# Optimization experiments

Measured on AMD Instinct MI355X. Metric: run time of the kernel, lower is better.

## Reference

```python
import jax, jax.numpy as jnp
import numpy as np

WS = 6          # window size
NUM_HEADS = 6
HEAD_DIM = 32   # dim=192 / 6 heads
SCALE = HEAD_DIM ** -0.5


def _rel_pos_index(ws):
    # Faithful to the torch buffer construction (torch.meshgrid default 'ij').
    coords = np.stack(np.meshgrid(np.arange(ws), np.arange(ws), np.arange(ws), indexing='ij'))  # [3,ws,ws,ws]
    flat = coords.reshape(3, -1)                       # [3, ws^3]
    rel = flat[:, :, None] - flat[:, None, :]          # [3, N, N]
    rel = rel.transpose(1, 2, 0).astype(np.int64)      # [N, N, 3]
    rel += ws - 1
    rel[..., 0] *= 3 * ws - 1
    rel[..., 1] *= 2 * ws - 1
    return rel.sum(-1)                                 # [N, N]

REL_INDEX = jnp.asarray(_rel_pos_index(WS))            # [216, 216] int


def setup_inputs() -> dict:
    key = jax.random.key(0)
    k1, k2, k3, k4 = jax.random.split(key, 4)
    B, N, C = 1024, WS ** 3, NUM_HEADS * HEAD_DIM
    return {
        "x": jax.random.normal(k1, (B, N, C), dtype=jnp.float32),
        "qkv_w": jax.random.normal(k2, (3 * C, C), dtype=jnp.float32) * 0.02,
        "proj_w": jax.random.normal(k3, (C, C), dtype=jnp.float32) * 0.02,
        "proj_b": jnp.zeros((C,), dtype=jnp.float32),
        "bias_table": jax.random.normal(k4, ((2 * WS - 1) ** 3, NUM_HEADS), dtype=jnp.float32) * 0.02,
    }


def reference(x, qkv_w, proj_w, proj_b, bias_table):
    B, N, C = x.shape
    H, D = NUM_HEADS, HEAD_DIM
    qkv = jnp.einsum('bnc,fc->bnf', x, qkv_w)              # [B,N,3C]
    qkv = qkv.reshape(B, N, 3, H, D).transpose(2, 0, 3, 1, 4)  # [3,B,H,N,D]
    q, k, v = qkv[0], qkv[1], qkv[2]
    attn = jnp.einsum('bhnd,bhmd->bhnm', q * SCALE, k)     # [B,H,N,N]
    bias = bias_table[REL_INDEX]                           # [N,N,H]
    attn = attn + bias.transpose(2, 0, 1)[None]            # add [1,H,N,N]
    attn = jax.nn.softmax(attn, axis=-1)
    out = jnp.einsum('bhnm,bhmd->bhnd', attn, v)           # [B,H,N,D]
    out = out.transpose(0, 2, 1, 3).reshape(B, N, C)
    return jnp.einsum('bnc,oc->bno', out, proj_w) + proj_b
```

## Files before the change

### kernel.cpp

```cpp
#include <hip/hip_runtime.h>
#include <cstdint>
#include <cstddef>


typedef __attribute__((ext_vector_type(8))) short short8;
typedef __attribute__((ext_vector_type(4))) float f32x4;

#define SCALE_F 0.17677669529663687f

__device__ __forceinline__ unsigned short f2bf(float f) {
  union { float f; unsigned u; } v; v.f = f;
  return (unsigned short)((v.u + 0x7fffu + ((v.u >> 16) & 1u)) >> 16);
}

__device__ __forceinline__ f32x4 mfma16(short8 a, short8 b, f32x4 c) {
  return __builtin_amdgcn_mfma_f32_16x16x32_bf16(a, b, c, 0, 0, 0);
}

__global__ void prep_kernel(const float* __restrict__ qkv_w,
                            const float* __restrict__ proj_w,
                            const float* __restrict__ bias_table,
                            unsigned short* __restrict__ wb,
                            unsigned short* __restrict__ pwb,
                            float* __restrict__ biasg) {
  const int tid = blockIdx.x * blockDim.x + threadIdx.x;
  const int stride = gridDim.x * blockDim.x;
  for (int i = tid; i < 576 * 192; i += stride) wb[i] = f2bf(qkv_w[i]);
  for (int i = tid; i < 192 * 192; i += stride) pwb[i] = f2bf(proj_w[i]);
  for (int i = tid; i < 6 * 216 * 216; i += stride) {
    const int h = i / 46656, rem = i % 46656;
    const int n = rem / 216, m = rem % 216;
    const int di = n / 36 - m / 36;
    const int dj = (n / 6) % 6 - (m / 6) % 6;
    const int dk = n % 6 - m % 6;
    const int idx = (di + 5) * 17 + (dj + 5) * 11 + (dk + 5);
    biasg[i] = bias_table[idx * 6 + h];
  }
}

__global__ __launch_bounds__(1024, 4)
void attn_kernel(const float* __restrict__ x, const unsigned short* __restrict__ wb,
                 const float* __restrict__ biasg, float* __restrict__ outbuf) {
  extern __shared__ char smem[];
  unsigned short* xs  = (unsigned short*)(smem);
  unsigned short* qs  = (unsigned short*)(smem + 86400);
  unsigned short* ks  = (unsigned short*)(smem + 104320);
  unsigned short* vT  = (unsigned short*)(smem + 122240);
  unsigned short* pch = (unsigned short*)(smem + 137088);

  const int b = blockIdx.x;
  const int tid = threadIdx.x;
  const int wave = tid >> 6;
  const int lane = tid & 63;
  const int quad = lane >> 4;
  const int lcol = lane & 15;

  {
    const float4* xg4 = (const float4*)(x + (size_t)b * 41472);
    for (int i = tid; i < 216 * 48; i += 1024) {
      const int row = i / 48, c4 = i % 48;
      const float4 v = xg4[row * 48 + c4];
      union { unsigned short s[4]; unsigned long long u; } pk;
      pk.s[0] = f2bf(v.x); pk.s[1] = f2bf(v.y);
      pk.s[2] = f2bf(v.z); pk.s[3] = f2bf(v.w);
      *(unsigned long long*)(xs + row * 200 + c4 * 4) = pk.u;
    }
    for (int i = tid; i < 8 * 40; i += 1024) { qs[216 * 40 + i] = 0; ks[216 * 40 + i] = 0; }
    for (int i = tid; i < 32 * 8; i += 1024) vT[(i >> 3) * 232 + 216 + (i & 7)] = 0;
  }
  __syncthreads();

  unsigned short* attnb = (unsigned short*)(outbuf + (size_t)b * 41472);

  for (int h = 0; h < 6; ++h) {
    for (int u = wave; u < 14; u += 16) {
      const int mtp = u >> 1;
      const int nh  = u & 1;
      f32x4 acc[2][3] = {};
#pragma unroll
      for (int kk = 0; kk < 6; ++kk) {
        const short8 a0 = *(const short8*)(xs + (mtp * 32      + lcol) * 200 + kk * 32 + quad * 8);
        const short8 a1 = *(const short8*)(xs + (mtp * 32 + 16 + lcol) * 200 + kk * 32 + quad * 8);
#pragma unroll
        for (int j = 0; j < 3; ++j) {
          const int nt = nh * 3 + j;
          const int fbase = (nt >> 1) * 192 + h * 32 + (nt & 1) * 16;
          const short8 bf = *(const short8*)(wb + (fbase + lcol) * 192 + kk * 32 + quad * 8);
          acc[0][j] = mfma16(a0, bf, acc[0][j]);
          acc[1][j] = mfma16(a1, bf, acc[1][j]);
        }
      }
#pragma unroll
      for (int mi = 0; mi < 2; ++mi) {
        const int nbase = (mtp * 2 + mi) * 16 + quad * 4;
#pragma unroll
        for (int j = 0; j < 3; ++j) {
          const int nt = nh * 3 + j;
#pragma unroll
          for (int r = 0; r < 4; ++r) {
            const int n = nbase + r;
            if (n < 216) {
              const unsigned short val = f2bf(acc[mi][j][r]);
              if (nt < 2)      qs[n * 40 + (nt & 1) * 16 + lcol] = val;
              else if (nt < 4) ks[n * 40 + (nt & 1) * 16 + lcol] = val;
              else             vT[((nt & 1) * 16 + lcol) * 232 + n] = val;
            }
          }
        }
      }
    }
    __syncthreads();

    if (wave < 14) {
      const int s = wave;
      unsigned short* pw_ = pch + wave * 640;
      const short8 qa = *(const short8*)(qs + (s * 16 + lcol) * 40 + quad * 8);
      f32x4 o0 = {}, o1 = {}, rsum = {};
      for (int mt2 = 0; mt2 < 7; ++mt2) {
        const short8 kb0 = *(const short8*)(ks + (mt2 * 32      + lcol) * 40 + quad * 8);
        const short8 kb1 = *(const short8*)(ks + (mt2 * 32 + 16 + lcol) * 40 + quad * 8);
        const f32x4 zero = {};
        const f32x4 s0 = mfma16(qa, kb0, zero);
        const f32x4 s1 = mfma16(qa, kb1, zero);
        const int nb = s * 16 + quad * 4;
#pragma unroll
        for (int t = 0; t < 2; ++t) {
          const int m = mt2 * 32 + t * 16 + lcol;
#pragma unroll
          for (int r = 0; r < 4; ++r) {
            const int n = nb + r;
            const int nc = (n < 216) ? n : 0;
            float p = 0.0f;
            if (m < 216)
              p = __expf((t ? s1[r] : s0[r]) * SCALE_F + biasg[(h * 216 + nc) * 216 + m]);
            rsum[r] += p;
            pw_[(quad * 4 + r) * 40 + t * 16 + lcol] = f2bf(p);
          }
        }
        __builtin_amdgcn_s_waitcnt(0);
        const short8 pa  = *(const short8*)(pw_ + lcol * 40 + quad * 8);
        const short8 vb0 = *(const short8*)(vT + lcol * 232        + mt2 * 32 + quad * 8);
        const short8 vb1 = *(const short8*)(vT + (16 + lcol) * 232 + mt2 * 32 + quad * 8);
        o0 = mfma16(pa, vb0, o0);
        o1 = mfma16(pa, vb1, o1);
      }
      f32x4 inv;
#pragma unroll
      for (int r = 0; r < 4; ++r) {
        float ssum = rsum[r];
        ssum += __shfl_xor(ssum, 1, 16);
        ssum += __shfl_xor(ssum, 2, 16);
        ssum += __shfl_xor(ssum, 4, 16);
        ssum += __shfl_xor(ssum, 8, 16);
        inv[r] = 1.0f / ssum;
      }
#pragma unroll
      for (int t = 0; t < 2; ++t) {
#pragma unroll
        for (int r = 0; r < 4; ++r) {
          const int n = s * 16 + quad * 4 + r;
          if (n < 216)
            attnb[n * 192 + h * 32 + t * 16 + lcol] = f2bf((t ? o1[r] : o0[r]) * inv[r]);
        }
      }
    }
    __syncthreads();
  }
}

__global__ __launch_bounds__(512, 2)
void proj_kernel(const unsigned short* __restrict__ pw, const float* __restrict__ proj_b,
                 float* __restrict__ outbuf) {
  extern __shared__ char smem[];
  unsigned short* as = (unsigned short*)smem;
  const int b = blockIdx.x, tid = threadIdx.x;
  const int wave = tid >> 6, lane = tid & 63, quad = lane >> 4, lcol = lane & 15;
  float* myout = outbuf + (size_t)b * 41472;
  const unsigned short* attnb = (const unsigned short*)myout;

  for (int i = tid; i < 216 * 24; i += 512) {
    const int row = i / 24, c8 = i % 24;
    *(short8*)(as + row * 200 + c8 * 8) = *(const short8*)(attnb + row * 192 + c8 * 8);
  }
  __syncthreads();

  for (int u = wave; u < 14; u += 8) {
    short8 a[6];
#pragma unroll
    for (int kk = 0; kk < 6; ++kk)
      a[kk] = *(const short8*)(as + (u * 16 + lcol) * 200 + kk * 32 + quad * 8);
    for (int nt = 0; nt < 12; ++nt) {
      f32x4 acc = {};
#pragma unroll
      for (int kk = 0; kk < 6; ++kk) {
        const short8 bf = *(const short8*)(pw + (nt * 16 + lcol) * 192 + kk * 32 + quad * 8);
        acc = mfma16(a[kk], bf, acc);
      }
      const float pbv = proj_b[nt * 16 + lcol];
      const int nb = u * 16 + quad * 4;
#pragma unroll
      for (int r = 0; r < 4; ++r) {
        const int n = nb + r;
        if (n < 216) myout[n * 192 + nt * 16 + lcol] = acc[r] + pbv;
      }
    }
  }
}

extern "C" void kernel_launch(void* const* d_in, const int* in_sizes, int n_in,
                              void* d_out, int out_size, void* d_ws, size_t ws_size,
                              hipStream_t stream) {
  (void)in_sizes; (void)n_in; (void)out_size; (void)ws_size;
  const float* x          = (const float*)d_in[0];
  const float* qkv_w      = (const float*)d_in[1];
  const float* proj_w     = (const float*)d_in[2];
  const float* proj_b     = (const float*)d_in[3];
  const float* bias_table = (const float*)d_in[4];
  float* out = (float*)d_out;

  unsigned short* wb  = (unsigned short*)d_ws;
  unsigned short* pwb = (unsigned short*)((char*)d_ws + 221184);
  float* biasg        = (float*)((char*)d_ws + 294912);

  (void)hipFuncSetAttribute((const void*)attn_kernel,
                            hipFuncAttributeMaxDynamicSharedMemorySize, 157568);
  (void)hipFuncSetAttribute((const void*)proj_kernel,
                            hipFuncAttributeMaxDynamicSharedMemorySize, 89600);

  prep_kernel<<<dim3(256), dim3(256), 0, stream>>>(qkv_w, proj_w, bias_table, wb, pwb, biasg);
  attn_kernel<<<dim3(1024), dim3(1024), 157568, stream>>>(x, wb, biasg, out);
  proj_kernel<<<dim3(1024), dim3(512), 89600, stream>>>(pwb, proj_b, out);
}
```

Measured before the change: 929.2 us.

## Pack bias as bf16 in MFMA layout, restructure QKV tiling and stage proj weights

Precomputes the relative position bias as bf16 in a layout that matches the MFMA output fragment, with masked columns set to -inf. Each attention wave can then load its bias with a few vector loads instead of many scattered fp32 gathers and skip the bounds checks. The QKV projection now uses one 16-row tile per wave with six output tiles and packed 32-bit stores, and V columns are permuted so P·V reads line up. The projection kernel stages its bf16 weights in padded LDS and runs with 1024 threads. Rounding the bias to bf16 adds a small precision loss, and the larger LDS use may lower occupancy.

Result: faster. 811.7 us (-12.6%).

```diff
diff --git a/kernel.cpp b/kernel.cpp
--- a/kernel.cpp
+++ b/kernel.cpp
@@ -5,12 +5,25 @@
 
 typedef __attribute__((ext_vector_type(8))) short short8;
 typedef __attribute__((ext_vector_type(4))) float f32x4;
+typedef unsigned short u16;
+typedef unsigned int   u32;
 
 #define SCALE_F 0.17677669529663687f
 
-__device__ __forceinline__ unsigned short f2bf(float f) {
-  union { float f; unsigned u; } v; v.f = f;
-  return (unsigned short)((v.u + 0x7fffu + ((v.u >> 16) & 1u)) >> 16);
+#define XS_OFF   0
+#define QS_OFF   89600
+#define KS_OFF   107520
+#define VT_OFF   125440
+#define PCH_OFF  140288
+#define ATTN_LDS 158208
+
+#define PROJ_AS_OFF  0
+#define PROJ_PW_OFF  86400
+#define PROJ_LDS     163200
+
+__device__ __forceinline__ u16 f2bf(float f) {
+  union { float f; u32 u; } v; v.f = f;
+  return (u16)((v.u + 0x7fffu + ((v.u >> 16) & 1u)) >> 16);
 }
 
 __device__ __forceinline__ f32x4 mfma16(short8 a, short8 b, f32x4 c) {
@@ -20,33 +33,44 @@
 __global__ void prep_kernel(const float* __restrict__ qkv_w,
                             const float* __restrict__ proj_w,
                             const float* __restrict__ bias_table,
-                            unsigned short* __restrict__ wb,
-                            unsigned short* __restrict__ pwb,
-                            float* __restrict__ biasg) {
+                            u16* __restrict__ wb,
+                            u16* __restrict__ pwb,
+                            u16* __restrict__ biasp) {
   const int tid = blockIdx.x * blockDim.x + threadIdx.x;
   const int stride = gridDim.x * blockDim.x;
   for (int i = tid; i < 576 * 192; i += stride) wb[i] = f2bf(qkv_w[i]);
   for (int i = tid; i < 192 * 192; i += stride) pwb[i] = f2bf(proj_w[i]);
-  for (int i = tid; i < 6 * 216 * 216; i += stride) {
-    const int h = i / 46656, rem = i % 46656;
-    const int n = rem / 216, m = rem % 216;
-    const int di = n / 36 - m / 36;
-    const int dj = (n / 6) % 6 - (m / 6) % 6;
-    const int dk = n % 6 - m % 6;
-    const int idx = (di + 5) * 17 + (dj + 5) * 11 + (dk + 5);
-    biasg[i] = bias_table[idx * 6 + h];
+  for (int i = tid; i < 6 * 7 * 16 * 224 * 2; i += stride) {
+    const int t = i & 1;
+    int j = i >> 1;
+    const int n = j % 224; j /= 224;
+    const int l = j & 15;  j >>= 4;
+    const int c = j % 7;
+    const int h = j / 7;
+    const int m = c * 32 + t * 16 + l;
+    u16 val;
+    if (n >= 216)      val = 0;
+    else if (m >= 216) val = 0xFF80;
+    else {
+      const int di = n / 36 - m / 36;
+      const int dj = (n / 6) % 6 - (m / 6) % 6;
+      const int dk = n % 6 - m % 6;
+      const int idx = (di + 5) * 17 + (dj + 5) * 11 + (dk + 5);
+      val = f2bf(bias_table[idx * 6 + h]);
+    }
+    biasp[i] = val;
   }
 }
 
 __global__ __launch_bounds__(1024, 4)
-void attn_kernel(const float* __restrict__ x, const unsigned short* __restrict__ wb,
-                 const float* __restrict__ biasg, float* __restrict__ outbuf) {
+void attn_kernel(const float* __restrict__ x, const u16* __restrict__ wb,
+                 const u16* __restrict__ biasp, float* __restrict__ outbuf) {
   extern __shared__ char smem[];
-  unsigned short* xs  = (unsigned short*)(smem);
-  unsigned short* qs  = (unsigned short*)(smem + 86400);
-  unsigned short* ks  = (unsigned short*)(smem + 104320);
-  unsigned short* vT  = (unsigned short*)(smem + 122240);
-  unsigned short* pch = (unsigned short*)(smem + 137088);
+  u16* xs  = (u16*)(smem + XS_OFF);
+  u16* qs  = (u16*)(smem + QS_OFF);
+  u16* ks  = (u16*)(smem + KS_OFF);
+  u16* vT  = (u16*)(smem + VT_OFF);
+  u16* pch = (u16*)(smem + PCH_OFF);
 
   const int b = blockIdx.x;
   const int tid = threadIdx.x;
@@ -60,52 +84,46 @@
     for (int i = tid; i < 216 * 48; i += 1024) {
       const int row = i / 48, c4 = i % 48;
       const float4 v = xg4[row * 48 + c4];
-      union { unsigned short s[4]; unsigned long long u; } pk;
+      union { u16 s[4]; unsigned long long u; } pk;
       pk.s[0] = f2bf(v.x); pk.s[1] = f2bf(v.y);
       pk.s[2] = f2bf(v.z); pk.s[3] = f2bf(v.w);
       *(unsigned long long*)(xs + row * 200 + c4 * 4) = pk.u;
     }
     for (int i = tid; i < 8 * 40; i += 1024) { qs[216 * 40 + i] = 0; ks[216 * 40 + i] = 0; }
-    for (int i = tid; i < 32 * 8; i += 1024) vT[(i >> 3) * 232 + 216 + (i & 7)] = 0;
+    for (int i = tid; i < 32 * 8; i += 1024) {
+      const int d = i >> 3, jj = i & 7;
+      vT[d * 232 + 209 + 2 * jj] = 0;
+    }
   }
   __syncthreads();
 
-  unsigned short* attnb = (unsigned short*)(outbuf + (size_t)b * 41472);
+  u16* attnb = (u16*)(outbuf + (size_t)b * 41472);
 
   for (int h = 0; h < 6; ++h) {
     for (int u = wave; u < 14; u += 16) {
-      const int mtp = u >> 1;
-      const int nh  = u & 1;
-      f32x4 acc[2][3] = {};
+      f32x4 acc[6] = {};
 #pragma unroll
       for (int kk = 0; kk < 6; ++kk) {
-        const short8 a0 = *(const short8*)(xs + (mtp * 32      + lcol) * 200 + kk * 32 + quad * 8);
-        const short8 a1 = *(const short8*)(xs + (mtp * 32 + 16 + lcol) * 200 + kk * 32 + quad * 8);
-#pragma unroll
-        for (int j = 0; j < 3; ++j) {
-          const int nt = nh * 3 + j;
-          const int fbase = (nt >> 1) * 192 + h * 32 + (nt & 1) * 16;
+        const short8 a = *(const short8*)(xs + (u * 16 + lcol) * 200 + kk * 32 + quad * 8);
+#pragma unroll
+        for (int j = 0; j < 6; ++j) {
+          const int fbase = (j >> 1) * 192 + h * 32 + (j & 1) * 16;
           const short8 bf = *(const short8*)(wb + (fbase + lcol) * 192 + kk * 32 + quad * 8);
-          acc[0][j] = mfma16(a0, bf, acc[0][j]);
-          acc[1][j] = mfma16(a1, bf, acc[1][j]);
-        }
-      }
-#pragma unroll
-      for (int mi = 0; mi < 2; ++mi) {
-        const int nbase = (mtp * 2 + mi) * 16 + quad * 4;
-#pragma unroll
-        for (int j = 0; j < 3; ++j) {
-          const int nt = nh * 3 + j;
-#pragma unroll
-          for (int r = 0; r < 4; ++r) {
-            const int n = nbase + r;
-            if (n < 216) {
-              const unsigned short val = f2bf(acc[mi][j][r]);
-              if (nt < 2)      qs[n * 40 + (nt & 1) * 16 + lcol] = val;
-              else if (nt < 4) ks[n * 40 + (nt & 1) * 16 + lcol] = val;
-              else             vT[((nt & 1) * 16 + lcol) * 232 + n] = val;
-            }
-          }
+          acc[j] = mfma16(a, bf, acc[j]);
+        }
+      }
+      const int nb = u * 16 + quad * 4;
+#pragma unroll
+      for (int r = 0; r < 4; ++r) {
+        const int n = nb + r;
+        if (n < 216) {
+          *(u32*)(qs + n * 40 + 2 * lcol) =
+              (u32)f2bf(acc[0][r]) | ((u32)f2bf(acc[1][r]) << 16);
+          *(u32*)(ks + n * 40 + 2 * lcol) =
+              (u32)f2bf(acc[2][r]) | ((u32)f2bf(acc[3][r]) << 16);
+          const int pm = (n & ~31) | (2 * (n & 15)) | ((n >> 4) & 1);
+          vT[lcol * 232 + pm]        = f2bf(acc[4][r]);
+          vT[(16 + lcol) * 232 + pm] = f2bf(acc[5][r]);
         }
       }
     }
@@ -113,37 +131,51 @@
 
     if (wave < 14) {
       const int s = wave;
-      unsigned short* pw_ = pch + wave * 640;
+      u16* pw_ = pch + wave * 640;
+
+      uint4 bias_q[7];
+#pragma unroll
+      for (int c = 0; c < 7; ++c)
+        bias_q[c] = *(const uint4*)(biasp + ((size_t)((h * 7 + c) * 16 + lcol)) * 448
+                                    + (s * 16 + quad * 4) * 2);
       const short8 qa = *(const short8*)(qs + (s * 16 + lcol) * 40 + quad * 8);
-      f32x4 o0 = {}, o1 = {}, rsum = {};
-      for (int mt2 = 0; mt2 < 7; ++mt2) {
-        const short8 kb0 = *(const short8*)(ks + (mt2 * 32      + lcol) * 40 + quad * 8);
-        const short8 kb1 = *(const short8*)(ks + (mt2 * 32 + 16 + lcol) * 40 + quad * 8);
-        const f32x4 zero = {};
-        const f32x4 s0 = mfma16(qa, kb0, zero);
-        const f32x4 s1 = mfma16(qa, kb1, zero);
-        const int nb = s * 16 + quad * 4;
-#pragma unroll
-        for (int t = 0; t < 2; ++t) {
-          const int m = mt2 * 32 + t * 16 + lcol;
-#pragma unroll
-          for (int r = 0; r < 4; ++r) {
-            const int n = nb + r;
-            const int nc = (n < 216) ? n : 0;
-            float p = 0.0f;
-            if (m < 216)
-              p = __expf((t ? s1[r] : s0[r]) * SCALE_F + biasg[(h * 216 + nc) * 216 + m]);
-            rsum[r] += p;
-            pw_[(quad * 4 + r) * 40 + t * 16 + lcol] = f2bf(p);
-          }
-        }
+
+      u32 pP[7][4];
+      f32x4 rsum = {};
+#pragma unroll
+      for (int c = 0; c < 7; ++c) {
+        const short8 kb0 = *(const short8*)(ks + (c * 32 + lcol) * 40 + quad * 8);
+        const short8 kb1 = *(const short8*)(ks + (c * 32 + 16 + lcol) * 40 + quad * 8);
+        const f32x4 z = {};
+        const f32x4 s0 = mfma16(qa, kb0, z);
+        const f32x4 s1 = mfma16(qa, kb1, z);
+        const u32* bw = (const u32*)&bias_q[c];
+#pragma unroll
+        for (int r = 0; r < 4; ++r) {
+          union { u32 u; float f; } b0, b1;
+          b0.u = bw[r] << 16;
+          b1.u = bw[r] & 0xFFFF0000u;
+          const float p0 = __expf(__builtin_fmaf(s0[r], SCALE_F, b0.f));
+          const float p1 = __expf(__builtin_fmaf(s1[r], SCALE_F, b1.f));
+          rsum[r] += p0 + p1;
+          pP[c][r] = (u32)f2bf(p0) | ((u32)f2bf(p1) << 16);
+        }
+      }
+
+      f32x4 o0 = {}, o1 = {};
+#pragma unroll
+      for (int c = 0; c < 7; ++c) {
+#pragma unroll
+        for (int r = 0; r < 4; ++r)
+          *(u32*)(pw_ + (quad * 4 + r) * 40 + 2 * lcol) = pP[c][r];
         __builtin_amdgcn_s_waitcnt(0);
         const short8 pa  = *(const short8*)(pw_ + lcol * 40 + quad * 8);
-        const short8 vb0 = *(const short8*)(vT + lcol * 232        + mt2 * 32 + quad * 8);
-        const short8 vb1 = *(const short8*)(vT + (16 + lcol) * 232 + mt2 * 32 + quad * 8);
+        const short8 vb0 = *(const short8*)(vT + lcol * 232 + c * 32 + quad * 8);
+        const short8 vb1 = *(const short8*)(vT + (16 + lcol) * 232 + c * 32 + quad * 8);
         o0 = mfma16(pa, vb0, o0);
         o1 = mfma16(pa, vb1, o1);
       }
+
       f32x4 inv;
 #pragma unroll
       for (int r = 0; r < 4; ++r) {
@@ -155,12 +187,11 @@
         inv[r] = 1.0f / ssum;
       }
 #pragma unroll
-      for (int t = 0; t < 2; ++t) {
-#pragma unroll
-        for (int r = 0; r < 4; ++r) {
-          const int n = s * 16 + quad * 4 + r;
-          if (n < 216)
-            attnb[n * 192 + h * 32 + t * 16 + lcol] = f2bf((t ? o1[r] : o0[r]) * inv[r]);
+      for (int r = 0; r < 4; ++r) {
+        const int n = s * 16 + quad * 4 + r;
+        if (n < 216) {
+          attnb[n * 192 + h * 32 + lcol]      = f2bf(o0[r] * inv[r]);
+          attnb[n * 192 + h * 32 + 16 + lcol] = f2bf(o1[r] * inv[r]);
         }
       }
     }
@@ -168,32 +199,41 @@
   }
 }
 
-__global__ __launch_bounds__(512, 2)
-void proj_kernel(const unsigned short* __restrict__ pw, const float* __restrict__ proj_b,
+__global__ __launch_bounds__(1024, 4)
+void proj_kernel(const u16* __restrict__ pwb, const float* __restrict__ proj_b,
                  float* __restrict__ outbuf) {
   extern __shared__ char smem[];
-  unsigned short* as = (unsigned short*)smem;
+  u16* as  = (u16*)(smem + PROJ_AS_OFF);
+  u16* pws = (u16*)(smem + PROJ_PW_OFF);
   const int b = blockIdx.x, tid = threadIdx.x;
   const int wave = tid >> 6, lane = tid & 63, quad = lane >> 4, lcol = lane & 15;
   float* myout = outbuf + (size_t)b * 41472;
-  const unsigned short* attnb = (const unsigned short*)myout;
-
-  for (int i = tid; i < 216 * 24; i += 512) {
+  const u16* attnb = (const u16*)myout;
+
+  for (int i = tid; i < 216 * 24; i += 1024) {
     const int row = i / 24, c8 = i % 24;
     *(short8*)(as + row * 200 + c8 * 8) = *(const short8*)(attnb + row * 192 + c8 * 8);
   }
+  for (int i = tid; i < 192 * 24; i += 1024) {
+    const int row = i / 24, c8 = i % 24;
+    *(short8*)(pws + row * 200 + c8 * 8) = *(const short8*)(pwb + row * 192 + c8 * 8);
+  }
   __syncthreads();
 
-  for (int u = wave; u < 14; u += 8) {
+  for (int u = wave; u < 14; u += 16) {
+    const int arow = u * 16 + lcol;
+    const bool ok = arow < 216;
     short8 a[6];
 #pragma unroll
-    for (int kk = 0; kk < 6; ++kk)
-      a[kk] = *(const short8*)(as + (u * 16 + lcol) * 200 + kk * 32 + quad * 8);
+    for (int kk = 0; kk < 6; ++kk) {
+      const short8 z = {};
+      a[kk] = ok ? *(const short8*)(as + arow * 200 + kk * 32 + quad * 8) : z;
+    }
     for (int nt = 0; nt < 12; ++nt) {
       f32x4 acc = {};
 #pragma unroll
       for (int kk = 0; kk < 6; ++kk) {
-        const short8 bf = *(const short8*)(pw + (nt * 16 + lcol) * 192 + kk * 32 + quad * 8);
+        const short8 bf = *(const short8*)(pws + (nt * 16 + lcol) * 200 + kk * 32 + quad * 8);
         acc = mfma16(a[kk], bf, acc);
       }
       const float pbv = proj_b[nt * 16 + lcol];
@@ -218,16 +258,16 @@
   const float* bias_table = (const float*)d_in[4];
   float* out = (float*)d_out;
 
-  unsigned short* wb  = (unsigned short*)d_ws;
-  unsigned short* pwb = (unsigned short*)((char*)d_ws + 221184);
-  float* biasg        = (float*)((char*)d_ws + 294912);
+  u16* wb    = (u16*)d_ws;
+  u16* pwb   = (u16*)((char*)d_ws + 221184);
+  u16* biasp = (u16*)((char*)d_ws + 294912);
 
   (void)hipFuncSetAttribute((const void*)attn_kernel,
-                            hipFuncAttributeMaxDynamicSharedMemorySize, 157568);
+                            hipFuncAttributeMaxDynamicSharedMemorySize, ATTN_LDS);
   (void)hipFuncSetAttribute((const void*)proj_kernel,
-                            hipFuncAttributeMaxDynamicSharedMemorySize, 89600);
-
-  prep_kernel<<<dim3(256), dim3(256), 0, stream>>>(qkv_w, proj_w, bias_table, wb, pwb, biasg);
-  attn_kernel<<<dim3(1024), dim3(1024), 157568, stream>>>(x, wb, biasg, out);
-  proj_kernel<<<dim3(1024), dim3(512), 89600, stream>>>(pwb, proj_b, out);
-}
+                            hipFuncAttributeMaxDynamicSharedMemorySize, PROJ_LDS);
+
+  prep_kernel<<<dim3(512), dim3(256), 0, stream>>>(qkv_w, proj_w, bias_table, wb, pwb, biasp);
+  attn_kernel<<<dim3(1024), dim3(1024), ATTN_LDS, stream>>>(x, wb, biasp, out);
+  proj_kernel<<<dim3(1024), dim3(1024), PROJ_LDS, stream>>>(pwb, proj_b, out);
+}
```
